# Optimization experiments

Measured on AMD Instinct MI355X. Metric: run time of the kernel, lower is better.

## Reference

```python
import jax, jax.numpy as jnp
import numpy as np

NUM_HEADS = 8
NUM_POINTS = 4
NUM_PIP = 4  # num_points_in_pillar
RADIUS = 0.12


def grid_sample_bilinear(feat, grid):
    """torch.nn.functional.grid_sample(mode='bilinear', padding_mode='zeros', align_corners=False).
    feat: [G, D, H, W], grid: [G, Q, P, 2] in [-1, 1] (x=width, y=height) -> [G, Q, P, D]."""
    G, D, H, W = feat.shape
    Q, P = grid.shape[1], grid.shape[2]
    x = (grid[..., 0] + 1.0) * 0.5 * W - 0.5
    y = (grid[..., 1] + 1.0) * 0.5 * H - 0.5
    x0 = jnp.floor(x)
    y0 = jnp.floor(y)
    feat_flat = feat.reshape(G, D, H * W).transpose(0, 2, 1)  # [G, HW, D]
    out = jnp.zeros((G, Q * P, D), dtype=feat.dtype)
    for dx, dy in ((0, 0), (1, 0), (0, 1), (1, 1)):
        xi = x0 + dx
        yi = y0 + dy
        w = (1.0 - jnp.abs(x - xi)) * (1.0 - jnp.abs(y - yi))
        valid = (xi >= 0) & (xi <= W - 1) & (yi >= 0) & (yi <= H - 1)
        xi_c = jnp.clip(xi, 0, W - 1).astype(jnp.int32)
        yi_c = jnp.clip(yi, 0, H - 1).astype(jnp.int32)
        idx = (yi_c * W + xi_c).reshape(G, Q * P)
        g = jnp.take_along_axis(feat_flat, idx[:, :, None], axis=1)  # [G, Q*P, D]
        out = out + g * (w * valid.astype(w.dtype)).reshape(G, Q * P, 1)
    return out.reshape(G, Q, P, D)


def setup_inputs() -> dict:
    key = jax.random.key(0)
    ks = jax.random.split(key, 8)
    B, N, C = 1, 2500, 256
    cams, H, W = 6, 46, 80
    return {
        "query": jax.random.normal(ks[0], (B, N, C), dtype=jnp.float32),
        "image_feats": jax.random.normal(ks[1], (B, cams, C, H, W), dtype=jnp.float32),
        "reference_points_cam": jax.random.uniform(ks[2], (B, cams, N, NUM_PIP, 2), dtype=jnp.float32),
        "bev_mask": jax.random.uniform(ks[3], (B, cams, N, NUM_PIP)) > 0.3,
        "offset_w": jax.random.normal(ks[4], (NUM_HEADS * NUM_PIP * NUM_POINTS * 2, C), dtype=jnp.float32) * 0.02,
        "offset_b": jnp.zeros((NUM_HEADS * NUM_PIP * NUM_POINTS * 2,), dtype=jnp.float32),
        "weight_w": jax.random.normal(ks[5], (NUM_HEADS * NUM_PIP * NUM_POINTS, C), dtype=jnp.float32) * 0.02,
        "weight_b": jnp.zeros((NUM_HEADS * NUM_PIP * NUM_POINTS,), dtype=jnp.float32),
        "out_w": jax.random.normal(ks[6], (C, C), dtype=jnp.float32) * 0.02,
        "out_b": jnp.zeros((C,), dtype=jnp.float32),
    }


def reference(query, image_feats, reference_points_cam, bev_mask,
              offset_w, offset_b, weight_w, weight_b, out_w, out_b):
    B, N, C = query.shape
    cams, H, W = image_feats.shape[1], image_feats.shape[3], image_feats.shape[4]
    heads, PiP, P = NUM_HEADS, NUM_PIP, NUM_POINTS
    K = PiP * P
    D = C // heads

    # Per-query learned offsets and attention logits
    offsets = jnp.tanh(query @ offset_w.T + offset_b).reshape(B, N, heads, PiP, P, 2) * RADIUS
    wl = (query @ weight_w.T + weight_b).reshape(B, N, heads, K)  # [B,N,h,K]

    # Sampling locations per camera: ref [B,cams,N,PiP,2] + offsets -> [B,cams,N,h,K,2]
    loc = reference_points_cam[:, :, :, None, :, None, :] + offsets[:, None]
    loc = loc.reshape(B, cams, N, heads, K, 2)

    # Visibility mask broadcast to points: [B,cams,N,h,K]
    vis = jnp.broadcast_to(bev_mask[:, :, :, None, :, None], (B, cams, N, heads, PiP, P))
    vis = vis.reshape(B, cams, N, heads, K)

    # Masked softmax over K (handles fully-masked rows)
    m = vis.astype(wl.dtype)
    logits = jnp.where(vis, wl[:, None], jnp.asarray(-1e9, wl.dtype))
    w = jax.nn.softmax(logits, axis=-1) * m
    w = w / jnp.clip(jnp.sum(w, axis=-1, keepdims=True), 1e-6)

    # grid_sample over all (batch, cam, head) at once
    grid = loc.transpose(0, 1, 3, 2, 4, 5).reshape(B * cams * heads, N, K, 2) * 2.0 - 1.0
    feat = image_feats.reshape(B * cams * heads, D, H, W)
    sampled = grid_sample_bilinear(feat, grid)  # [B*cams*h, N, K, D]
    sampled = sampled.reshape(B, cams, heads, N, K, D).transpose(0, 1, 3, 2, 4, 5)  # [B,cams,N,h,K,D]

    cam_out = jnp.sum(sampled * w[..., None], axis=4).reshape(B, cams, N, C)

    has_vis = jnp.any(bev_mask, axis=-1)  # [B,cams,N]
    cam_out = cam_out * has_vis[..., None].astype(cam_out.dtype)

    fused = jnp.sum(cam_out, axis=1)  # [B,N,C]
    counts = jnp.clip(jnp.sum(has_vis.astype(jnp.int32), axis=1), 1)  # [B,N]
    fused = fused / counts[..., None].astype(fused.dtype)
    return fused @ out_w.T + out_b
```

## Files before the change

### kernel.cpp

```cpp
#include <hip/hip_runtime.h>
#include <math.h>

#define CAMS 6
#define CCH 256
#define HH 46
#define WW 80
#define NPIX (HH * WW)
#define HEADS 8
#define PIP 4
#define PP 4
#define KK 16
#define RADIUS_F 0.12f
#define NC 384
#define FEATB (58 * 4 * CAMS)
#define QTB (40 * 4)

__device__ __forceinline__ unsigned short f2bf(float f) {
    unsigned int x = __float_as_uint(f);
    unsigned int r = (x + 0x7FFFu + ((x >> 16) & 1u)) >> 16;
    return (unsigned short)r;
}
__device__ __forceinline__ float bf2f(unsigned short u) {
    return __uint_as_float(((unsigned int)u) << 16);
}

__global__ void __launch_bounds__(256) prep2_k(const float* __restrict__ imfeat,
                                               unsigned short* __restrict__ feat_t,
                                               const float* __restrict__ offw,
                                               const float* __restrict__ ww,
                                               const float* __restrict__ outw,
                                               const float* __restrict__ query,
                                               float* __restrict__ WCi,
                                               float* __restrict__ outTi,
                                               float* __restrict__ qTi,
                                               int N) {
    __shared__ float tile[64][65];
    int b = blockIdx.x;
    int tj = threadIdx.x & 63;
    int ti = threadIdx.x >> 6;
    if (b < FEATB) {
        int px = b % 58, rest = b / 58;
        int r0 = (rest % 4) * 64;
        int cam = rest / 4;
        int p0 = px * 64;
        const float* src = imfeat + ((long)cam * CCH + r0) * NPIX + p0;
#pragma unroll
        for (int k = 0; k < 64; k += 4) {
            if (p0 + tj < NPIX) tile[ti + k][tj] = src[(long)(ti + k) * NPIX + tj];
        }
        __syncthreads();
        unsigned short* dst = feat_t + ((long)cam * NPIX + p0) * CCH + r0;
#pragma unroll
        for (int k = 0; k < 64; k += 4) {
            if (p0 + ti + k < NPIX) dst[(long)(ti + k) * CCH + tj] = f2bf(tile[tj][ti + k]);
        }
    } else if (b < FEATB + 40) {
        int c = b - FEATB;
        const float* src;
        float* dst;
        int tr, tc, dcols, dcol0;
        if (c < 16)      { src = offw; dst = WCi;   tr = c >> 2;        tc = c & 3;         dcols = NC;  dcol0 = 0; }
        else if (c < 24) { src = ww;   dst = WCi;   tr = (c - 16) & 1;  tc = (c - 16) >> 1; dcols = NC;  dcol0 = 256; }
        else             { src = outw; dst = outTi; tr = (c - 24) >> 2; tc = (c - 24) & 3;  dcols = 256; dcol0 = 0; }
#pragma unroll
        for (int k = 0; k < 64; k += 4)
            tile[ti + k][tj] = src[(long)(tr * 64 + ti + k) * CCH + tc * 64 + tj];
        __syncthreads();
        int col = dcol0 + tr * 64 + tj;
#pragma unroll
        for (int q = ti; q < 16; q += 4) {
            float4 v = make_float4(tile[tj][4 * q + 0], tile[tj][4 * q + 1],
                                   tile[tj][4 * q + 2], tile[tj][4 * q + 3]);
            ((float4*)dst)[(long)(tc * 16 + q) * dcols + col] = v;
        }
    } else {
        int c = b - FEATB - 40;
        int nt = c % 40, ct = c / 40;
        int n0 = nt * 64, c0 = ct * 64;
#pragma unroll
        for (int k = 0; k < 64; k += 4) {
            int row = ti + k;
            tile[row][tj] = (n0 + row < N) ? query[(long)(n0 + row) * CCH + c0 + tj] : 0.f;
        }
        __syncthreads();
        int n = n0 + tj;
        if (n < N) {
#pragma unroll
            for (int q = ti; q < 16; q += 4) {
                float4 v = make_float4(tile[tj][4 * q + 0], tile[tj][4 * q + 1],
                                       tile[tj][4 * q + 2], tile[tj][4 * q + 3]);
                ((float4*)qTi)[(long)((c0 >> 2) + q) * N + n] = v;
            }
        }
    }
}

__global__ void __launch_bounds__(256) qgemm7_k(const float* __restrict__ qTi,
                                                const float* __restrict__ WCi,
                                                const float* __restrict__ offB,
                                                const float* __restrict__ wB,
                                                float* __restrict__ offsets,
                                                float* __restrict__ wl,
                                                int N) {
    int n = blockIdx.x * 256 + threadIdx.x;
    int col0 = blockIdx.y * 8;
    int nc = min(n, N - 1);
    const float4* ap = (const float4*)qTi + nc;
    const float4* wp = (const float4*)WCi + col0;
    float acc[8] = {0.f, 0.f, 0.f, 0.f, 0.f, 0.f, 0.f, 0.f};
#pragma unroll 4
    for (int kg = 0; kg < 64; kg++) {
        float4 a = ap[(long)kg * N];
#pragma unroll
        for (int j = 0; j < 8; j++) {
            float4 wv = wp[(long)kg * NC + j];
            acc[j] = fmaf(a.w, wv.w, fmaf(a.z, wv.z, fmaf(a.y, wv.y, fmaf(a.x, wv.x, acc[j]))));
        }
    }
    if (n < N) {
        if (col0 < 256) {
#pragma unroll
            for (int j = 0; j < 8; j++)
                offsets[(long)n * CCH + col0 + j] = tanhf(acc[j] + offB[col0 + j]) * RADIUS_F;
        } else {
#pragma unroll
            for (int j = 0; j < 8; j++)
                wl[(long)n * 128 + (col0 - 256) + j] = acc[j] + wB[(col0 - 256) + j];
        }
    }
}

__global__ void __launch_bounds__(256, 4) sample_cam_k(
        const unsigned short* __restrict__ feat_t,
        const float* __restrict__ refp,
        const int* __restrict__ bev,
        const float* __restrict__ offsets,
        const float* __restrict__ wl,
        float* __restrict__ cam_out,
        int N, int per_xcd) {
    int xcd = blockIdx.x & 7;
    int local = (blockIdx.x >> 3) * 4 + (threadIdx.x >> 6);
    if (local >= per_xcd) return;
    long task = (long)xcd * per_xcd + local;
    if (task >= (long)CAMS * N) return;
    int cam = (int)(task / N);
    int n = (int)(task - (long)cam * N);

    int l = threadIdx.x & 63;
    int h = l >> 3;

    const int* bv = bev + ((long)cam * N + n) * 4;
    int m0 = bv[0], m1 = bv[1], m2 = bv[2], m3 = bv[3];
    float* outp = cam_out + ((long)cam * N + n) * CCH + (l << 2);
    if (!(m0 | m1 | m2 | m3)) {
        *(float4*)outp = make_float4(0.f, 0.f, 0.f, 0.f);
        return;
    }

    const float* rp = refp + ((long)cam * N + n) * 8;
    const float4* offn = (const float4*)(offsets + (long)n * CCH + (h << 5));
    const float4* wln = (const float4*)(wl + (long)n * 128 + (h << 4));

    float4 wl0, wl1, wl2, wl3;
    float mmax = -1e30f;
    if (m0) { wl0 = wln[0]; mmax = fmaxf(mmax, fmaxf(fmaxf(wl0.x, wl0.y), fmaxf(wl0.z, wl0.w))); }
    if (m1) { wl1 = wln[1]; mmax = fmaxf(mmax, fmaxf(fmaxf(wl1.x, wl1.y), fmaxf(wl1.z, wl1.w))); }
    if (m2) { wl2 = wln[2]; mmax = fmaxf(mmax, fmaxf(fmaxf(wl2.x, wl2.y), fmaxf(wl2.z, wl2.w))); }
    if (m3) { wl3 = wln[3]; mmax = fmaxf(mmax, fmaxf(fmaxf(wl3.x, wl3.y), fmaxf(wl3.z, wl3.w))); }

    float w_[KK];
#pragma unroll
    for (int k = 0; k < KK; k++) w_[k] = 0.f;
    float ssum = 0.f;
    if (m0) {
        w_[0] = __expf(wl0.x - mmax); w_[1] = __expf(wl0.y - mmax);
        w_[2] = __expf(wl0.z - mmax); w_[3] = __expf(wl0.w - mmax);
        ssum += w_[0] + w_[1] + w_[2] + w_[3];
    }
    if (m1) {
        w_[4] = __expf(wl1.x - mmax); w_[5] = __expf(wl1.y - mmax);
        w_[6] = __expf(wl1.z - mmax); w_[7] = __expf(wl1.w - mmax);
        ssum += w_[4] + w_[5] + w_[6] + w_[7];
    }
    if (m2) {
        w_[8] = __expf(wl2.x - mmax); w_[9] = __expf(wl2.y - mmax);
        w_[10] = __expf(wl2.z - mmax); w_[11] = __expf(wl2.w - mmax);
        ssum += w_[8] + w_[9] + w_[10] + w_[11];
    }
    if (m3) {
        w_[12] = __expf(wl3.x - mmax); w_[13] = __expf(wl3.y - mmax);
        w_[14] = __expf(wl3.z - mmax); w_[15] = __expf(wl3.w - mmax);
        ssum += w_[12] + w_[13] + w_[14] + w_[15];
    }
    float inv = 1.f / ssum;

    const ushort4* fcam = (const ushort4*)(feat_t + (long)cam * NPIX * CCH) + l;
    float ax = 0.f, ay = 0.f, az = 0.f, aw = 0.f;

#pragma unroll
    for (int pip = 0; pip < PIP; pip++) {
        int vis = (pip == 0) ? m0 : (pip == 1) ? m1 : (pip == 2) ? m2 : m3;
        if (!vis) continue;
        float rx = rp[pip * 2 + 0];
        float ry = rp[pip * 2 + 1];
        float4 oa = offn[pip * 2];
        float4 ob = offn[pip * 2 + 1];
        float px[PP] = {oa.x, oa.z, ob.x, ob.z};
        float py[PP] = {oa.y, oa.w, ob.y, ob.w};
#pragma unroll
        for (int p = 0; p < PP; p++) {
            float wgt = w_[pip * PP + p];
            float x = fmaf(rx + px[p], (float)WW, -0.5f);
            float y = fmaf(ry + py[p], (float)HH, -0.5f);
            float x0f = floorf(x), y0f = floorf(y);
            float fx = x - x0f, fy = y - y0f;
            int ix = (int)x0f, iy = (int)y0f;
            int ix0 = min(max(ix, 0), WW - 1);
            int ix1 = min(max(ix + 1, 0), WW - 1);
            int iy0 = min(max(iy, 0), HH - 1);
            int iy1 = min(max(iy + 1, 0), HH - 1);
            float wx0 = (1.f - fx) * (((ix >= 0) & (ix < WW)) ? 1.f : 0.f);
            float wx1 = fx * (((ix + 1 >= 0) & (ix + 1 < WW)) ? 1.f : 0.f);
            float wy0 = (1.f - fy) * (((iy >= 0) & (iy < HH)) ? 1.f : 0.f);
            float wy1 = fy * (((iy + 1 >= 0) & (iy + 1 < HH)) ? 1.f : 0.f);
            const ushort4 u00 = fcam[(iy0 * WW + ix0) * (CCH / 4)];
            const ushort4 u01 = fcam[(iy0 * WW + ix1) * (CCH / 4)];
            const ushort4 u10 = fcam[(iy1 * WW + ix0) * (CCH / 4)];
            const ushort4 u11 = fcam[(iy1 * WW + ix1) * (CCH / 4)];
            float a00 = wgt * wy0 * wx0;
            float a01 = wgt * wy0 * wx1;
            float a10 = wgt * wy1 * wx0;
            float a11 = wgt * wy1 * wx1;
            ax = fmaf(a00, bf2f(u00.x), ax); ay = fmaf(a00, bf2f(u00.y), ay);
            az = fmaf(a00, bf2f(u00.z), az); aw = fmaf(a00, bf2f(u00.w), aw);
            ax = fmaf(a01, bf2f(u01.x), ax); ay = fmaf(a01, bf2f(u01.y), ay);
            az = fmaf(a01, bf2f(u01.z), az); aw = fmaf(a01, bf2f(u01.w), aw);
            ax = fmaf(a10, bf2f(u10.x), ax); ay = fmaf(a10, bf2f(u10.y), ay);
            az = fmaf(a10, bf2f(u10.z), az); aw = fmaf(a10, bf2f(u10.w), aw);
            ax = fmaf(a11, bf2f(u11.x), ax); ay = fmaf(a11, bf2f(u11.y), ay);
            az = fmaf(a11, bf2f(u11.z), az); aw = fmaf(a11, bf2f(u11.w), aw);
        }
    }
    *(float4*)outp = make_float4(ax * inv, ay * inv, az * inv, aw * inv);
}

__global__ void __launch_bounds__(256) camsum_t_k(const float* __restrict__ cam_out,
                                                  float* __restrict__ fsumTi, int N) {
    __shared__ float4 lds[16][33];
    int t = threadIdx.x;
    int n0 = blockIdx.x * 32;
    int kg0 = blockIdx.y * 16;
    const float4* src = (const float4*)cam_out;
#pragma unroll
    for (int pass = 0; pass < 2; pass++) {
        int item = t + pass * 256;
        int row = item >> 4;
        int c = item & 15;
        int n = n0 + row;
        float4 s = make_float4(0.f, 0.f, 0.f, 0.f);
        if (n < N) {
#pragma unroll
            for (int cam = 0; cam < CAMS; cam++) {
                float4 v = src[((long)cam * N + n) * 64 + kg0 + c];
                s.x += v.x; s.y += v.y; s.z += v.z; s.w += v.w;
            }
        }
        lds[c][row] = s;
    }
    __syncthreads();
    float4* dst = (float4*)fsumTi;
#pragma unroll
    for (int pass = 0; pass < 2; pass++) {
        int item = t + pass * 256;
        int k = item >> 5;
        int row = item & 31;
        int n = n0 + row;
        if (n < N) dst[(long)(kg0 + k) * N + n] = lds[k][row];
    }
}

__global__ void __launch_bounds__(256) outproj7_k(const float* __restrict__ fsumTi,
                                                  const int* __restrict__ bev,
                                                  const float* __restrict__ outTi,
                                                  const float* __restrict__ outB,
                                                  float* __restrict__ out, int N) {
    int n = blockIdx.x * 256 + threadIdx.x;
    int col0 = blockIdx.y * 8;
    int nc = min(n, N - 1);
    const float4* ap = (const float4*)fsumTi + nc;
    const float4* wp = (const float4*)outTi + col0;
    const int4* bv4 = (const int4*)bev;
    int cnt = 0;
#pragma unroll
    for (int cam = 0; cam < CAMS; cam++) {
        int4 bv = bv4[(long)cam * N + nc];
        cnt += (bv.x | bv.y | bv.z | bv.w) ? 1 : 0;
    }
    float inv = 1.f / (float)max(cnt, 1);
    float acc[8] = {0.f, 0.f, 0.f, 0.f, 0.f, 0.f, 0.f, 0.f};
#pragma unroll 4
    for (int kg = 0; kg < 64; kg++) {
        float4 a = ap[(long)kg * N];
#pragma unroll
        for (int j = 0; j < 8; j++) {
            float4 wv = wp[(long)kg * CCH + j];
            acc[j] = fmaf(a.w, wv.w, fmaf(a.z, wv.z, fmaf(a.y, wv.y, fmaf(a.x, wv.x, acc[j]))));
        }
    }
    if (n < N) {
#pragma unroll
        for (int j = 0; j < 8; j++)
            out[(long)n * CCH + col0 + j] = fmaf(acc[j], inv, outB[col0 + j]);
    }
}

extern "C" void kernel_launch(void* const* d_in, const int* in_sizes, int n_in,
                              void* d_out, int out_size, void* d_ws, size_t ws_size,
                              hipStream_t stream) {
    const float* query    = (const float*)d_in[0];
    const float* imfeat   = (const float*)d_in[1];
    const float* refp     = (const float*)d_in[2];
    const int*   bev      = (const int*)d_in[3];
    const float* offset_w = (const float*)d_in[4];
    const float* offset_b = (const float*)d_in[5];
    const float* weight_w = (const float*)d_in[6];
    const float* weight_b = (const float*)d_in[7];
    const float* out_w    = (const float*)d_in[8];
    const float* out_b    = (const float*)d_in[9];
    float* out = (float*)d_out;

    int N = in_sizes[0] / CCH;

    float* ws = (float*)d_ws;
    unsigned short* feat_t = (unsigned short*)ws;
    float* WCi    = ws + (size_t)CAMS * NPIX * CCH / 2;
    float* outTi  = WCi + (size_t)CCH * NC;
    float* offs   = outTi + (size_t)CCH * CCH;
    float* wl     = offs + (size_t)N * CCH;
    float* camob  = wl + (size_t)N * 128;
    float* qTi    = camob + (size_t)CAMS * N * CCH;
    float* fsumTi = qTi + (size_t)64 * N * 4;

    prep2_k<<<FEATB + 40 + QTB, 256, 0, stream>>>(imfeat, feat_t, offset_w, weight_w,
                                                  out_w, query, WCi, outTi, qTi, N);

    int nblk = (N + 255) / 256;
    qgemm7_k<<<dim3(nblk, 48), 256, 0, stream>>>(qTi, WCi, offset_b, weight_b,
                                                 offs, wl, N);

    int T = CAMS * N;
    int per_xcd = (T + 7) / 8;
    int blocks = 8 * ((per_xcd + 3) / 4);
    sample_cam_k<<<blocks, 256, 0, stream>>>(feat_t, refp, bev, offs, wl, camob,
                                             N, per_xcd);

    camsum_t_k<<<dim3((N + 31) / 32, 4), 256, 0, stream>>>(camob, fsumTi, N);

    outproj7_k<<<dim3(nblk, 32), 256, 0, stream>>>(fsumTi, bev, outTi, out_b, out, N);
}
```

Measured before the change: 90.66 us.

## Restructure projection GEMMs with LDS-staged query tiles and column-quad weight layout

The two small GEMMs (query projection and output projection) are rewritten so each block stages a 16-row tile of the transposed activations in LDS. Each thread computes a 2-row by 4-column output patch, reading weights from a new column-quad interleaved layout written by the prep kernel. Outputs are stored as float4 vectors. The aim is to replace per-thread strided global activation loads and scalar stores with LDS reuse and coalesced vector I/O. In exchange the grid becomes many small blocks, and the visibility count is recomputed per output row.

```diff
diff --git a/kernel.cpp b/kernel.cpp
--- a/kernel.cpp
+++ b/kernel.cpp
@@ -24,7 +24,7 @@
     return __uint_as_float(((unsigned int)u) << 16);
 }
 
-__global__ void __launch_bounds__(256) prep2_k(const float* __restrict__ imfeat,
+__global__ void __launch_bounds__(256) prep3_k(const float* __restrict__ imfeat,
                                                unsigned short* __restrict__ feat_t,
                                                const float* __restrict__ offw,
                                                const float* __restrict__ ww,
@@ -58,10 +58,10 @@
         int c = b - FEATB;
         const float* src;
         float* dst;
-        int tr, tc, dcols, dcol0;
-        if (c < 16)      { src = offw; dst = WCi;   tr = c >> 2;        tc = c & 3;         dcols = NC;  dcol0 = 0; }
-        else if (c < 24) { src = ww;   dst = WCi;   tr = (c - 16) & 1;  tc = (c - 16) >> 1; dcols = NC;  dcol0 = 256; }
-        else             { src = outw; dst = outTi; tr = (c - 24) >> 2; tc = (c - 24) & 3;  dcols = 256; dcol0 = 0; }
+        int tr, tc, dcol0, CQ;
+        if (c < 16)      { src = offw; dst = WCi;   tr = c >> 2;        tc = c & 3;         dcol0 = 0;   CQ = 96; }
+        else if (c < 24) { src = ww;   dst = WCi;   tr = (c - 16) & 1;  tc = (c - 16) >> 1; dcol0 = 256; CQ = 96; }
+        else             { src = outw; dst = outTi; tr = (c - 24) >> 2; tc = (c - 24) & 3;  dcol0 = 0;   CQ = 64; }
 #pragma unroll
         for (int k = 0; k < 64; k += 4)
             tile[ti + k][tj] = src[(long)(tr * 64 + ti + k) * CCH + tc * 64 + tj];
@@ -71,7 +71,8 @@
         for (int q = ti; q < 16; q += 4) {
             float4 v = make_float4(tile[tj][4 * q + 0], tile[tj][4 * q + 1],
                                    tile[tj][4 * q + 2], tile[tj][4 * q + 3]);
-            ((float4*)dst)[(long)(tc * 16 + q) * dcols + col] = v;
+            int kg = tc * 16 + q;
+            ((float4*)dst)[((long)kg * CQ + (col >> 2)) * 4 + (col & 3)] = v;
         }
     } else {
         int c = b - FEATB - 40;
@@ -95,37 +96,78 @@
     }
 }
 
-__global__ void __launch_bounds__(256) qgemm7_k(const float* __restrict__ qTi,
-                                                const float* __restrict__ WCi,
-                                                const float* __restrict__ offB,
-                                                const float* __restrict__ wB,
-                                                float* __restrict__ offsets,
-                                                float* __restrict__ wl,
-                                                int N) {
-    int n = blockIdx.x * 256 + threadIdx.x;
-    int col0 = blockIdx.y * 8;
-    int nc = min(n, N - 1);
-    const float4* ap = (const float4*)qTi + nc;
-    const float4* wp = (const float4*)WCi + col0;
-    float acc[8] = {0.f, 0.f, 0.f, 0.f, 0.f, 0.f, 0.f, 0.f};
+__global__ void __launch_bounds__(256) qgemm11_k(const float* __restrict__ qTi,
+                                                 const float* __restrict__ WCi,
+                                                 const float* __restrict__ offB,
+                                                 const float* __restrict__ wB,
+                                                 float* __restrict__ offsets,
+                                                 float* __restrict__ wl,
+                                                 int N) {
+    __shared__ float4 a_lds[64][16];
+    int t = threadIdx.x;
+    int n0 = blockIdx.x * 16;
+    int colg = blockIdx.y;
+
+    const float4* qt4 = (const float4*)qTi;
+#pragma unroll
+    for (int i = 0; i < 4; i++) {
+        int idx = t + i * 256;
+        int kg = idx >> 4, nn = idx & 15;
+        int n = n0 + nn;
+        a_lds[kg][nn] = (n < N) ? qt4[(long)kg * N + n] : make_float4(0.f, 0.f, 0.f, 0.f);
+    }
+    __syncthreads();
+
+    int cq = t & 31;
+    int ng = t >> 5;
+    int cqg = colg * 32 + cq;
+    const float4* wp = (const float4*)WCi + (long)cqg * 4;
+
+    float acc0x = 0.f, acc0y = 0.f, acc0z = 0.f, acc0w = 0.f;
+    float acc1x = 0.f, acc1y = 0.f, acc1z = 0.f, acc1w = 0.f;
 #pragma unroll 4
     for (int kg = 0; kg < 64; kg++) {
-        float4 a = ap[(long)kg * N];
-#pragma unroll
-        for (int j = 0; j < 8; j++) {
-            float4 wv = wp[(long)kg * NC + j];
-            acc[j] = fmaf(a.w, wv.w, fmaf(a.z, wv.z, fmaf(a.y, wv.y, fmaf(a.x, wv.x, acc[j]))));
-        }
-    }
-    if (n < N) {
-        if (col0 < 256) {
-#pragma unroll
-            for (int j = 0; j < 8; j++)
-                offsets[(long)n * CCH + col0 + j] = tanhf(acc[j] + offB[col0 + j]) * RADIUS_F;
-        } else {
-#pragma unroll
-            for (int j = 0; j < 8; j++)
-                wl[(long)n * 128 + (col0 - 256) + j] = acc[j] + wB[(col0 - 256) + j];
+        float4 a0 = a_lds[kg][2 * ng];
+        float4 a1 = a_lds[kg][2 * ng + 1];
+        const float4* wk = wp + (long)kg * (96 * 4);
+        float4 w0 = wk[0];
+        float4 w1 = wk[1];
+        float4 w2 = wk[2];
+        float4 w3 = wk[3];
+        acc0x = fmaf(a0.w, w0.w, fmaf(a0.z, w0.z, fmaf(a0.y, w0.y, fmaf(a0.x, w0.x, acc0x))));
+        acc0y = fmaf(a0.w, w1.w, fmaf(a0.z, w1.z, fmaf(a0.y, w1.y, fmaf(a0.x, w1.x, acc0y))));
+        acc0z = fmaf(a0.w, w2.w, fmaf(a0.z, w2.z, fmaf(a0.y, w2.y, fmaf(a0.x, w2.x, acc0z))));
+        acc0w = fmaf(a0.w, w3.w, fmaf(a0.z, w3.z, fmaf(a0.y, w3.y, fmaf(a0.x, w3.x, acc0w))));
+        acc1x = fmaf(a1.w, w0.w, fmaf(a1.z, w0.z, fmaf(a1.y, w0.y, fmaf(a1.x, w0.x, acc1x))));
+        acc1y = fmaf(a1.w, w1.w, fmaf(a1.z, w1.z, fmaf(a1.y, w1.y, fmaf(a1.x, w1.x, acc1y))));
+        acc1z = fmaf(a1.w, w2.w, fmaf(a1.z, w2.z, fmaf(a1.y, w2.y, fmaf(a1.x, w2.x, acc1z))));
+        acc1w = fmaf(a1.w, w3.w, fmaf(a1.z, w3.z, fmaf(a1.y, w3.y, fmaf(a1.x, w3.x, acc1w))));
+    }
+
+    int col = cqg * 4;
+    int na = n0 + 2 * ng, nb = na + 1;
+    if (col < 256) {
+        float4 bb = *(const float4*)(offB + col);
+        if (na < N) {
+            float4 r = make_float4(tanhf(acc0x + bb.x) * RADIUS_F, tanhf(acc0y + bb.y) * RADIUS_F,
+                                   tanhf(acc0z + bb.z) * RADIUS_F, tanhf(acc0w + bb.w) * RADIUS_F);
+            *(float4*)(offsets + (long)na * CCH + col) = r;
+        }
+        if (nb < N) {
+            float4 r = make_float4(tanhf(acc1x + bb.x) * RADIUS_F, tanhf(acc1y + bb.y) * RADIUS_F,
+                                   tanhf(acc1z + bb.z) * RADIUS_F, tanhf(acc1w + bb.w) * RADIUS_F);
+            *(float4*)(offsets + (long)nb * CCH + col) = r;
+        }
+    } else {
+        int c2 = col - 256;
+        float4 bb = *(const float4*)(wB + c2);
+        if (na < N) {
+            float4 r = make_float4(acc0x + bb.x, acc0y + bb.y, acc0z + bb.z, acc0w + bb.w);
+            *(float4*)(wl + (long)na * 128 + c2) = r;
+        }
+        if (nb < N) {
+            float4 r = make_float4(acc1x + bb.x, acc1y + bb.y, acc1z + bb.z, acc1w + bb.w);
+            *(float4*)(wl + (long)nb * 128 + c2) = r;
         }
     }
 }
@@ -279,38 +321,79 @@
     }
 }
 
-__global__ void __launch_bounds__(256) outproj7_k(const float* __restrict__ fsumTi,
-                                                  const int* __restrict__ bev,
-                                                  const float* __restrict__ outTi,
-                                                  const float* __restrict__ outB,
-                                                  float* __restrict__ out, int N) {
-    int n = blockIdx.x * 256 + threadIdx.x;
-    int col0 = blockIdx.y * 8;
-    int nc = min(n, N - 1);
-    const float4* ap = (const float4*)fsumTi + nc;
-    const float4* wp = (const float4*)outTi + col0;
-    const int4* bv4 = (const int4*)bev;
-    int cnt = 0;
-#pragma unroll
-    for (int cam = 0; cam < CAMS; cam++) {
-        int4 bv = bv4[(long)cam * N + nc];
-        cnt += (bv.x | bv.y | bv.z | bv.w) ? 1 : 0;
-    }
-    float inv = 1.f / (float)max(cnt, 1);
-    float acc[8] = {0.f, 0.f, 0.f, 0.f, 0.f, 0.f, 0.f, 0.f};
+__global__ void __launch_bounds__(256) outproj11_k(const float* __restrict__ fsumTi,
+                                                   const int* __restrict__ bev,
+                                                   const float* __restrict__ outTi,
+                                                   const float* __restrict__ outB,
+                                                   float* __restrict__ out, int N) {
+    __shared__ float4 a_lds[64][16];
+    int t = threadIdx.x;
+    int n0 = blockIdx.x * 16;
+    int colg = blockIdx.y;
+
+    const float4* ft4 = (const float4*)fsumTi;
+#pragma unroll
+    for (int i = 0; i < 4; i++) {
+        int idx = t + i * 256;
+        int kg = idx >> 4, nn = idx & 15;
+        int n = n0 + nn;
+        a_lds[kg][nn] = (n < N) ? ft4[(long)kg * N + n] : make_float4(0.f, 0.f, 0.f, 0.f);
+    }
+    __syncthreads();
+
+    int cq = t & 31;
+    int ng = t >> 5;
+    int cqg = colg * 32 + cq;
+    const float4* wp = (const float4*)outTi + (long)cqg * 4;
+
+    float acc0x = 0.f, acc0y = 0.f, acc0z = 0.f, acc0w = 0.f;
+    float acc1x = 0.f, acc1y = 0.f, acc1z = 0.f, acc1w = 0.f;
 #pragma unroll 4
     for (int kg = 0; kg < 64; kg++) {
-        float4 a = ap[(long)kg * N];
-#pragma unroll
-        for (int j = 0; j < 8; j++) {
-            float4 wv = wp[(long)kg * CCH + j];
-            acc[j] = fmaf(a.w, wv.w, fmaf(a.z, wv.z, fmaf(a.y, wv.y, fmaf(a.x, wv.x, acc[j]))));
-        }
-    }
-    if (n < N) {
-#pragma unroll
-        for (int j = 0; j < 8; j++)
-            out[(long)n * CCH + col0 + j] = fmaf(acc[j], inv, outB[col0 + j]);
+        float4 a0 = a_lds[kg][2 * ng];
+        float4 a1 = a_lds[kg][2 * ng + 1];
+        const float4* wk = wp + (long)kg * (64 * 4);
+        float4 w0 = wk[0];
+        float4 w1 = wk[1];
+        float4 w2 = wk[2];
+        float4 w3 = wk[3];
+        acc0x = fmaf(a0.w, w0.w, fmaf(a0.z, w0.z, fmaf(a0.y, w0.y, fmaf(a0.x, w0.x, acc0x))));
+        acc0y = fmaf(a0.w, w1.w, fmaf(a0.z, w1.z, fmaf(a0.y, w1.y, fmaf(a0.x, w1.x, acc0y))));
+        acc0z = fmaf(a0.w, w2.w, fmaf(a0.z, w2.z, fmaf(a0.y, w2.y, fmaf(a0.x, w2.x, acc0z))));
+        acc0w = fmaf(a0.w, w3.w, fmaf(a0.z, w3.z, fmaf(a0.y, w3.y, fmaf(a0.x, w3.x, acc0w))));
+        acc1x = fmaf(a1.w, w0.w, fmaf(a1.z, w0.z, fmaf(a1.y, w0.y, fmaf(a1.x, w0.x, acc1x))));
+        acc1y = fmaf(a1.w, w1.w, fmaf(a1.z, w1.z, fmaf(a1.y, w1.y, fmaf(a1.x, w1.x, acc1y))));
+        acc1z = fmaf(a1.w, w2.w, fmaf(a1.z, w2.z, fmaf(a1.y, w2.y, fmaf(a1.x, w2.x, acc1z))));
+        acc1w = fmaf(a1.w, w3.w, fmaf(a1.z, w3.z, fmaf(a1.y, w3.y, fmaf(a1.x, w3.x, acc1w))));
+    }
+
+    int col = cqg * 4;
+    int na = n0 + 2 * ng, nb = na + 1;
+    const int4* bv4 = (const int4*)bev;
+    float4 bb = *(const float4*)(outB + col);
+    if (na < N) {
+        int cnt = 0;
+#pragma unroll
+        for (int cam = 0; cam < CAMS; cam++) {
+            int4 bv = bv4[(long)cam * N + na];
+            cnt += (bv.x | bv.y | bv.z | bv.w) ? 1 : 0;
+        }
+        float inv = 1.f / (float)max(cnt, 1);
+        float4 r = make_float4(fmaf(acc0x, inv, bb.x), fmaf(acc0y, inv, bb.y),
+                               fmaf(acc0z, inv, bb.z), fmaf(acc0w, inv, bb.w));
+        *(float4*)(out + (long)na * CCH + col) = r;
+    }
+    if (nb < N) {
+        int cnt = 0;
+#pragma unroll
+        for (int cam = 0; cam < CAMS; cam++) {
+            int4 bv = bv4[(long)cam * N + nb];
+            cnt += (bv.x | bv.y | bv.z | bv.w) ? 1 : 0;
+        }
+        float inv = 1.f / (float)max(cnt, 1);
+        float4 r = make_float4(fmaf(acc1x, inv, bb.x), fmaf(acc1y, inv, bb.y),
+                               fmaf(acc1z, inv, bb.z), fmaf(acc1w, inv, bb.w));
+        *(float4*)(out + (long)nb * CCH + col) = r;
     }
 }
 
@@ -341,11 +424,11 @@
     float* qTi    = camob + (size_t)CAMS * N * CCH;
     float* fsumTi = qTi + (size_t)64 * N * 4;
 
-    prep2_k<<<FEATB + 40 + QTB, 256, 0, stream>>>(imfeat, feat_t, offset_w, weight_w,
+    prep3_k<<<FEATB + 40 + QTB, 256, 0, stream>>>(imfeat, feat_t, offset_w, weight_w,
                                                   out_w, query, WCi, outTi, qTi, N);
 
-    int nblk = (N + 255) / 256;
-    qgemm7_k<<<dim3(nblk, 48), 256, 0, stream>>>(qTi, WCi, offset_b, weight_b,
+    int nb16 = (N + 15) / 16;
+    qgemm11_k<<<dim3(nb16, 3), 256, 0, stream>>>(qTi, WCi, offset_b, weight_b,
                                                  offs, wl, N);
 
     int T = CAMS * N;
@@ -356,5 +439,5 @@
 
     camsum_t_k<<<dim3((N + 31) / 32, 4), 256, 0, stream>>>(camob, fsumTi, N);
 
-    outproj7_k<<<dim3(nblk, 32), 256, 0, stream>>>(fsumTi, bev, outTi, out_b, out, N);
-}
+    outproj11_k<<<dim3(nb16, 2), 256, 0, stream>>>(fsumTi, bev, outTi, out_b, out, N);
+}
```

New measurement: 118.1 us. +30.2%, slower.

## Retile query and output projection GEMMs with LDS-staged activations and coalesced columns

Applied to the files above, without the earlier changes.

Both small FP32 GEMMs switch from one-row-per-thread, 8-columns-per-block tiling to blocks that cover 16 rows and all output columns. Each block stages the activation tile in LDS and each thread computes 2 rows by 12 (or 8) strided columns. Consecutive threads now read consecutive weight columns and write contiguous outputs. This targets redundant activation reads across the many column-blocks and the uncoalesced stores, in exchange for more registers per thread and a grid of about 157 blocks, which may underfill the GPU.

```diff
diff --git a/kernel.cpp b/kernel.cpp
--- a/kernel.cpp
+++ b/kernel.cpp
@@ -95,38 +95,61 @@
     }
 }
 
-__global__ void __launch_bounds__(256) qgemm7_k(const float* __restrict__ qTi,
-                                                const float* __restrict__ WCi,
-                                                const float* __restrict__ offB,
-                                                const float* __restrict__ wB,
-                                                float* __restrict__ offsets,
-                                                float* __restrict__ wl,
-                                                int N) {
-    int n = blockIdx.x * 256 + threadIdx.x;
-    int col0 = blockIdx.y * 8;
-    int nc = min(n, N - 1);
-    const float4* ap = (const float4*)qTi + nc;
-    const float4* wp = (const float4*)WCi + col0;
-    float acc[8] = {0.f, 0.f, 0.f, 0.f, 0.f, 0.f, 0.f, 0.f};
-#pragma unroll 4
+__global__ void __launch_bounds__(256) qgemm12_k(const float* __restrict__ qTi,
+                                                 const float* __restrict__ WCi,
+                                                 const float* __restrict__ offB,
+                                                 const float* __restrict__ wB,
+                                                 float* __restrict__ offsets,
+                                                 float* __restrict__ wl,
+                                                 int N) {
+    __shared__ float4 a_lds[64][16];
+    int t = threadIdx.x;
+    int n0 = blockIdx.x * 16;
+    const float4* qt4 = (const float4*)qTi;
+#pragma unroll
+    for (int i = 0; i < 4; i++) {
+        int idx = t + i * 256;
+        int kg = idx >> 4, nn = idx & 15;
+        int n = n0 + nn;
+        a_lds[kg][nn] = (n < N) ? qt4[(long)kg * N + n] : make_float4(0.f, 0.f, 0.f, 0.f);
+    }
+    __syncthreads();
+
+    int cl = t & 31;
+    int np = t >> 5;
+    const float4* wp = (const float4*)WCi + cl;
+
+    float acc0[12], acc1[12];
+#pragma unroll
+    for (int j = 0; j < 12; j++) { acc0[j] = 0.f; acc1[j] = 0.f; }
+
+#pragma unroll 2
     for (int kg = 0; kg < 64; kg++) {
-        float4 a = ap[(long)kg * N];
-#pragma unroll
-        for (int j = 0; j < 8; j++) {
-            float4 wv = wp[(long)kg * NC + j];
-            acc[j] = fmaf(a.w, wv.w, fmaf(a.z, wv.z, fmaf(a.y, wv.y, fmaf(a.x, wv.x, acc[j]))));
-        }
-    }
-    if (n < N) {
-        if (col0 < 256) {
-#pragma unroll
-            for (int j = 0; j < 8; j++)
-                offsets[(long)n * CCH + col0 + j] = tanhf(acc[j] + offB[col0 + j]) * RADIUS_F;
-        } else {
-#pragma unroll
-            for (int j = 0; j < 8; j++)
-                wl[(long)n * 128 + (col0 - 256) + j] = acc[j] + wB[(col0 - 256) + j];
-        }
+        float4 a0 = a_lds[kg][2 * np];
+        float4 a1 = a_lds[kg][2 * np + 1];
+        const float4* wk = wp + (long)kg * NC;
+#pragma unroll
+        for (int j = 0; j < 12; j++) {
+            float4 wv = wk[32 * j];
+            acc0[j] = fmaf(a0.w, wv.w, fmaf(a0.z, wv.z, fmaf(a0.y, wv.y, fmaf(a0.x, wv.x, acc0[j]))));
+            acc1[j] = fmaf(a1.w, wv.w, fmaf(a1.z, wv.z, fmaf(a1.y, wv.y, fmaf(a1.x, wv.x, acc1[j]))));
+        }
+    }
+
+    int na = n0 + 2 * np, nb = na + 1;
+#pragma unroll
+    for (int j = 0; j < 8; j++) {
+        int col = cl + 32 * j;
+        float b = offB[col];
+        if (na < N) offsets[(long)na * CCH + col] = tanhf(acc0[j] + b) * RADIUS_F;
+        if (nb < N) offsets[(long)nb * CCH + col] = tanhf(acc1[j] + b) * RADIUS_F;
+    }
+#pragma unroll
+    for (int j = 8; j < 12; j++) {
+        int c2 = cl + 32 * j - 256;
+        float b = wB[c2];
+        if (na < N) wl[(long)na * 128 + c2] = acc0[j] + b;
+        if (nb < N) wl[(long)nb * 128 + c2] = acc1[j] + b;
     }
 }
 
@@ -279,38 +302,72 @@
     }
 }
 
-__global__ void __launch_bounds__(256) outproj7_k(const float* __restrict__ fsumTi,
-                                                  const int* __restrict__ bev,
-                                                  const float* __restrict__ outTi,
-                                                  const float* __restrict__ outB,
-                                                  float* __restrict__ out, int N) {
-    int n = blockIdx.x * 256 + threadIdx.x;
-    int col0 = blockIdx.y * 8;
-    int nc = min(n, N - 1);
-    const float4* ap = (const float4*)fsumTi + nc;
-    const float4* wp = (const float4*)outTi + col0;
+__global__ void __launch_bounds__(256) outproj12_k(const float* __restrict__ fsumTi,
+                                                   const int* __restrict__ bev,
+                                                   const float* __restrict__ outTi,
+                                                   const float* __restrict__ outB,
+                                                   float* __restrict__ out, int N) {
+    __shared__ float4 a_lds[64][16];
+    int t = threadIdx.x;
+    int n0 = blockIdx.x * 16;
+    const float4* ft4 = (const float4*)fsumTi;
+#pragma unroll
+    for (int i = 0; i < 4; i++) {
+        int idx = t + i * 256;
+        int kg = idx >> 4, nn = idx & 15;
+        int n = n0 + nn;
+        a_lds[kg][nn] = (n < N) ? ft4[(long)kg * N + n] : make_float4(0.f, 0.f, 0.f, 0.f);
+    }
+    __syncthreads();
+
+    int cl = t & 31;
+    int np = t >> 5;
+    const float4* wp = (const float4*)outTi + cl;
+
+    float acc0[8], acc1[8];
+#pragma unroll
+    for (int j = 0; j < 8; j++) { acc0[j] = 0.f; acc1[j] = 0.f; }
+
+#pragma unroll 2
+    for (int kg = 0; kg < 64; kg++) {
+        float4 a0 = a_lds[kg][2 * np];
+        float4 a1 = a_lds[kg][2 * np + 1];
+        const float4* wk = wp + (long)kg * 256;
+#pragma unroll
+        for (int j = 0; j < 8; j++) {
+            float4 wv = wk[32 * j];
+            acc0[j] = fmaf(a0.w, wv.w, fmaf(a0.z, wv.z, fmaf(a0.y, wv.y, fmaf(a0.x, wv.x, acc0[j]))));
+            acc1[j] = fmaf(a1.w, wv.w, fmaf(a1.z, wv.z, fmaf(a1.y, wv.y, fmaf(a1.x, wv.x, acc1[j]))));
+        }
+    }
+
+    int na = n0 + 2 * np, nb = na + 1;
     const int4* bv4 = (const int4*)bev;
-    int cnt = 0;
-#pragma unroll
-    for (int cam = 0; cam < CAMS; cam++) {
-        int4 bv = bv4[(long)cam * N + nc];
-        cnt += (bv.x | bv.y | bv.z | bv.w) ? 1 : 0;
-    }
-    float inv = 1.f / (float)max(cnt, 1);
-    float acc[8] = {0.f, 0.f, 0.f, 0.f, 0.f, 0.f, 0.f, 0.f};
-#pragma unroll 4
-    for (int kg = 0; kg < 64; kg++) {
-        float4 a = ap[(long)kg * N];
-#pragma unroll
-        for (int j = 0; j < 8; j++) {
-            float4 wv = wp[(long)kg * CCH + j];
-            acc[j] = fmaf(a.w, wv.w, fmaf(a.z, wv.z, fmaf(a.y, wv.y, fmaf(a.x, wv.x, acc[j]))));
-        }
-    }
-    if (n < N) {
-#pragma unroll
-        for (int j = 0; j < 8; j++)
-            out[(long)n * CCH + col0 + j] = fmaf(acc[j], inv, outB[col0 + j]);
+    float inva = 1.f, invb = 1.f;
+    if (na < N) {
+        int cnt = 0;
+#pragma unroll
+        for (int cam = 0; cam < CAMS; cam++) {
+            int4 bv = bv4[(long)cam * N + na];
+            cnt += (bv.x | bv.y | bv.z | bv.w) ? 1 : 0;
+        }
+        inva = 1.f / (float)max(cnt, 1);
+    }
+    if (nb < N) {
+        int cnt = 0;
+#pragma unroll
+        for (int cam = 0; cam < CAMS; cam++) {
+            int4 bv = bv4[(long)cam * N + nb];
+            cnt += (bv.x | bv.y | bv.z | bv.w) ? 1 : 0;
+        }
+        invb = 1.f / (float)max(cnt, 1);
+    }
+#pragma unroll
+    for (int j = 0; j < 8; j++) {
+        int col = cl + 32 * j;
+        float b = outB[col];
+        if (na < N) out[(long)na * CCH + col] = fmaf(acc0[j], inva, b);
+        if (nb < N) out[(long)nb * CCH + col] = fmaf(acc1[j], invb, b);
     }
 }
 
@@ -344,9 +401,8 @@
     prep2_k<<<FEATB + 40 + QTB, 256, 0, stream>>>(imfeat, feat_t, offset_w, weight_w,
                                                   out_w, query, WCi, outTi, qTi, N);
 
-    int nblk = (N + 255) / 256;
-    qgemm7_k<<<dim3(nblk, 48), 256, 0, stream>>>(qTi, WCi, offset_b, weight_b,
-                                                 offs, wl, N);
+    int nb16 = (N + 15) / 16;
+    qgemm12_k<<<nb16, 256, 0, stream>>>(qTi, WCi, offset_b, weight_b, offs, wl, N);
 
     int T = CAMS * N;
     int per_xcd = (T + 7) / 8;
@@ -356,5 +412,5 @@
 
     camsum_t_k<<<dim3((N + 31) / 32, 4), 256, 0, stream>>>(camob, fsumTi, N);
 
-    outproj7_k<<<dim3(nblk, 32), 256, 0, stream>>>(fsumTi, bev, outTi, out_b, out, N);
-}
+    outproj12_k<<<nb16, 256, 0, stream>>>(fsumTi, bev, outTi, out_b, out, N);
+}
```

Measured after the change: 113.6 us. 1.25x slower.
